# Kernel optimization log

Hardware: AMD Instinct MI355X
Metric: run time of the kernel (lower is better)

The kernel has to match this reference:

```python
import jax, jax.numpy as jnp
import numpy as np

N = 100000      # nodes
E = 3200000     # edges (avg degree 32)
IN_DIM = 256
OUT_DIM = 256


def setup_inputs() -> dict:
    key = jax.random.key(0)
    k1, k2, k3, k4, k5, k6 = jax.random.split(key, 6)
    row = jax.random.randint(k1, (E,), 0, N, dtype=jnp.int32)
    col = jax.random.randint(k2, (E,), 0, N, dtype=jnp.int32)
    vals = jax.random.uniform(k3, (E,), dtype=jnp.float32)
    x = jax.random.normal(k4, (N, IN_DIM), dtype=jnp.float32)
    W = jax.random.normal(k5, (IN_DIM, OUT_DIM), dtype=jnp.float32) * (IN_DIM ** -0.5)
    b = jax.random.normal(k6, (OUT_DIM,), dtype=jnp.float32) * 0.01
    return {"row": row, "col": col, "vals": vals, "x": x, "W": W, "b": b}


def reference(row, col, vals, x, W, b):
    # H = A_hat @ x  (sparse COO matmul via gather + segment-sum scatter)
    gathered = vals[:, None] * x[col]              # [E, in_dim]
    agg = jax.ops.segment_sum(gathered, row, num_segments=N)  # [N, in_dim]
    # Dense linear: agg @ W + b
    return agg @ W + b                             # [N, out_dim]
```

## Files before the change

### kernel.cpp

```cpp
#include <hip/hip_runtime.h>

#define IN_DIM 256
#define OUT_DIM 256
#define NBITS 8
#define CHUNK 8192
#define CAP 13056
#define VAL_SCALE 32767.0f
#define INV_VAL_SCALE (1.0f / 32767.0f)

typedef __attribute__((ext_vector_type(8))) short bf16x8;
typedef __attribute__((ext_vector_type(4))) float f32x4;

static __device__ __forceinline__ unsigned short f2bf(float f) {
    unsigned int u = __float_as_uint(f);
    u = (u + 0x7FFFu + ((u >> 16) & 1u)) >> 16;
    return (unsigned short)u;
}

__global__ __launch_bounds__(256) void prep_kernel(const float* __restrict__ W,
                                                   unsigned short* __restrict__ Wb,
                                                   int* __restrict__ cursor, int nb) {
    int blk = blockIdx.x;
    int t = threadIdx.x;
    if (blk < 256) {
        int idx = blk * 256 + t;
        int k = idx >> 8, c = idx & 255;
        Wb[(c >> 4) * 4096 + (k >> 3) * 128 + (c & 15) * 8 + (k & 7)] = f2bf(W[idx]);
    } else {
        for (int i = t; i < nb; i += 256) cursor[i] = i * CAP;
    }
}

__global__ __launch_bounds__(512) void gemm_scatter_fused(
        const float* __restrict__ x, const unsigned short* __restrict__ Wb,
        unsigned short* __restrict__ y, int M,
        const int* __restrict__ row, const int* __restrict__ col,
        const float* __restrict__ vals, int* __restrict__ cursor,
        unsigned int* __restrict__ edge_p, unsigned char* __restrict__ rowloc,
        int E, int nb, int GB) {
    __shared__ int hist[512];
    __shared__ int gbase[512];
    __shared__ int cur[512];

    if (blockIdx.x < (unsigned)GB) {
        const int t = threadIdx.x;
        const int lane = t & 63;
        const int wid = t >> 6;
        const int wr = wid >> 2;
        const int wc = wid & 3;
        const int r0 = blockIdx.x * 128 + wr * 64;
        const int c0 = wc * 64;

        f32x4 acc[4][4];
#pragma unroll
        for (int m = 0; m < 4; ++m)
#pragma unroll
            for (int n = 0; n < 4; ++n) acc[m][n] = (f32x4){0.f, 0.f, 0.f, 0.f};

        const int arow_off = lane & 15;
        const int kgrp = lane >> 4;

#pragma unroll
        for (int step = 0; step < 8; ++step) {
            const int k0 = step * 32 + kgrp * 8;
            bf16x8 a[4], bfr[4];
#pragma unroll
            for (int m = 0; m < 4; ++m) {
                int rr = r0 + m * 16 + arow_off;
                rr = min(rr, M - 1);
                const float* xr = x + (size_t)rr * IN_DIM + k0;
                float4 f0 = *reinterpret_cast<const float4*>(xr);
                float4 f1 = *reinterpret_cast<const float4*>(xr + 4);
                a[m][0] = (short)f2bf(f0.x); a[m][1] = (short)f2bf(f0.y);
                a[m][2] = (short)f2bf(f0.z); a[m][3] = (short)f2bf(f0.w);
                a[m][4] = (short)f2bf(f1.x); a[m][5] = (short)f2bf(f1.y);
                a[m][6] = (short)f2bf(f1.z); a[m][7] = (short)f2bf(f1.w);
            }
#pragma unroll
            for (int n = 0; n < 4; ++n) {
                int nbk = wc * 4 + n;
                bfr[n] = *reinterpret_cast<const bf16x8*>(
                    Wb + (size_t)nbk * 4096 + (step * 4 + kgrp) * 128 + arow_off * 8);
            }
#pragma unroll
            for (int m = 0; m < 4; ++m)
#pragma unroll
                for (int n = 0; n < 4; ++n)
                    acc[m][n] = __builtin_amdgcn_mfma_f32_16x16x32_bf16(a[m], bfr[n], acc[m][n], 0, 0, 0);
        }

#pragma unroll
        for (int m = 0; m < 4; ++m) {
            int rbase = r0 + m * 16 + kgrp * 4;
#pragma unroll
            for (int i = 0; i < 4; ++i) {
                int rr = rbase + i;
                if (rr < M) {
                    unsigned short* yr = y + (size_t)rr * OUT_DIM + c0 + arow_off;
#pragma unroll
                    for (int n = 0; n < 4; ++n) yr[n * 16] = f2bf(acc[m][n][i]);
                }
            }
        }
    } else {
        const int t = threadIdx.x;
        const int base_e = (blockIdx.x - GB) * CHUNK;
        for (int i = t; i < nb; i += 512) { hist[i] = 0; cur[i] = 0; }
        __syncthreads();
#pragma unroll
        for (int i = 0; i < CHUNK / 512; ++i) {
            int e = base_e + i * 512 + t;
            if (e < E) atomicAdd(&hist[row[e] >> NBITS], 1);
        }
        __syncthreads();
        for (int i = t; i < nb; i += 512) {
            int c = hist[i];
            if (c > 0) gbase[i] = atomicAdd(&cursor[i], c);
        }
        __syncthreads();
#pragma unroll
        for (int i = 0; i < CHUNK / 512; ++i) {
            int e = base_e + i * 512 + t;
            if (e < E) {
                int r = row[e];
                int bk = r >> NBITS;
                int loc = atomicAdd(&cur[bk], 1);
                int dest = gbase[bk] + loc;
                unsigned int vq = (unsigned int)(vals[e] * VAL_SCALE + 0.5f);
                edge_p[dest] = ((unsigned int)col[e] << 15) | vq;
                rowloc[dest] = (unsigned char)(r & 255);
            }
        }
    }
}

__global__ __launch_bounds__(512) void bucket_to_csr(const int* __restrict__ cursor,
                                                     unsigned int* __restrict__ edge_p,
                                                     const unsigned char* __restrict__ rowloc,
                                                     int2* __restrict__ row_se, int N, int nb) {
    __shared__ unsigned int ep[CAP];
    __shared__ unsigned char rl[CAP];
    __shared__ int cnt[256];
    __shared__ int cur[256];
    __shared__ int fin[256];
    __shared__ int wsum[4];
    const int t = threadIdx.x;
    const int b = blockIdx.x;
    const int gb = b * CAP;
    int m = cursor[b] - gb;
    if (m > CAP) m = CAP;
    if (t < 256) cnt[t] = 0;
    __syncthreads();
    for (int i = t; i < m; i += 512) {
        ep[i] = edge_p[gb + i];
        unsigned char r = rowloc[gb + i];
        rl[i] = r;
        atomicAdd(&cnt[r], 1);
    }
    __syncthreads();
    int pcv = 0, incl = 0;
    const int lane = t & 63;
    const int w = t >> 6;
    if (t < 256) {
        pcv = (cnt[t] + 3) & ~3;
        incl = pcv;
#pragma unroll
        for (int off = 1; off < 64; off <<= 1) {
            int u = __shfl_up(incl, off, 64);
            if (lane >= off) incl += u;
        }
        if (lane == 63) wsum[w] = incl;
    }
    __syncthreads();
    if (t < 256) {
        int wp = 0;
        for (int k = 0; k < w; ++k) wp += wsum[k];
        int excl = wp + incl - pcv;
        cur[t] = excl;
        fin[t] = excl + pcv;
        const int baseRow = b << NBITS;
        if (t < N - baseRow)
            row_se[baseRow + t] = make_int2(gb + excl, gb + excl + pcv);
    }
    __syncthreads();
    for (int i = t; i < m; i += 512) {
        int r = rl[i];
        int pos = atomicAdd(&cur[r], 1);
        edge_p[gb + pos] = ep[i];
    }
    __syncthreads();
    if (t < 256) {
        for (int pos = cur[t]; pos < fin[t]; ++pos)
            edge_p[gb + pos] = 0u;
    }
}

__global__ __launch_bounds__(256) void aggregate_rows_bf16(const int2* __restrict__ row_se,
                                                           const unsigned int* __restrict__ edge_p,
                                                           const unsigned short* __restrict__ y,
                                                           const float* __restrict__ b,
                                                           float* __restrict__ out, int N) {
    const int lane = threadIdx.x & 63;
    const int w = threadIdx.x >> 6;
    const int r = blockIdx.x * 4 + w;
    if (r >= N) return;

    const int2 se = row_se[r];
    const int start = se.x;
    const int end = se.y;
    const int half = lane >> 5;
    const int d0 = (lane & 31) * 8;

    float acc[8];
#pragma unroll
    for (int i = 0; i < 8; ++i) acc[i] = 0.f;

    int j = start;
    for (; j + 8 <= end; j += 8) {
        uint4 mp = *reinterpret_cast<const uint4*>(edge_p + j + half * 4);
        float v0 = (float)(mp.x & 0x7fffu) * INV_VAL_SCALE;
        float v1 = (float)(mp.y & 0x7fffu) * INV_VAL_SCALE;
        float v2 = (float)(mp.z & 0x7fffu) * INV_VAL_SCALE;
        float v3 = (float)(mp.w & 0x7fffu) * INV_VAL_SCALE;
        uint4 u0 = *reinterpret_cast<const uint4*>(y + ((size_t)(mp.x >> 15)) * OUT_DIM + d0);
        uint4 u1 = *reinterpret_cast<const uint4*>(y + ((size_t)(mp.y >> 15)) * OUT_DIM + d0);
        uint4 u2 = *reinterpret_cast<const uint4*>(y + ((size_t)(mp.z >> 15)) * OUT_DIM + d0);
        uint4 u3 = *reinterpret_cast<const uint4*>(y + ((size_t)(mp.w >> 15)) * OUT_DIM + d0);
        acc[0] += v0 * __uint_as_float(u0.x << 16);
        acc[1] += v0 * __uint_as_float(u0.x & 0xffff0000u);
        acc[2] += v0 * __uint_as_float(u0.y << 16);
        acc[3] += v0 * __uint_as_float(u0.y & 0xffff0000u);
        acc[4] += v0 * __uint_as_float(u0.z << 16);
        acc[5] += v0 * __uint_as_float(u0.z & 0xffff0000u);
        acc[6] += v0 * __uint_as_float(u0.w << 16);
        acc[7] += v0 * __uint_as_float(u0.w & 0xffff0000u);
        acc[0] += v1 * __uint_as_float(u1.x << 16);
        acc[1] += v1 * __uint_as_float(u1.x & 0xffff0000u);
        acc[2] += v1 * __uint_as_float(u1.y << 16);
        acc[3] += v1 * __uint_as_float(u1.y & 0xffff0000u);
        acc[4] += v1 * __uint_as_float(u1.z << 16);
        acc[5] += v1 * __uint_as_float(u1.z & 0xffff0000u);
        acc[6] += v1 * __uint_as_float(u1.w << 16);
        acc[7] += v1 * __uint_as_float(u1.w & 0xffff0000u);
        acc[0] += v2 * __uint_as_float(u2.x << 16);
        acc[1] += v2 * __uint_as_float(u2.x & 0xffff0000u);
        acc[2] += v2 * __uint_as_float(u2.y << 16);
        acc[3] += v2 * __uint_as_float(u2.y & 0xffff0000u);
        acc[4] += v2 * __uint_as_float(u2.z << 16);
        acc[5] += v2 * __uint_as_float(u2.z & 0xffff0000u);
        acc[6] += v2 * __uint_as_float(u2.w << 16);
        acc[7] += v2 * __uint_as_float(u2.w & 0xffff0000u);
        acc[0] += v3 * __uint_as_float(u3.x << 16);
        acc[1] += v3 * __uint_as_float(u3.x & 0xffff0000u);
        acc[2] += v3 * __uint_as_float(u3.y << 16);
        acc[3] += v3 * __uint_as_float(u3.y & 0xffff0000u);
        acc[4] += v3 * __uint_as_float(u3.z << 16);
        acc[5] += v3 * __uint_as_float(u3.z & 0xffff0000u);
        acc[6] += v3 * __uint_as_float(u3.w << 16);
        acc[7] += v3 * __uint_as_float(u3.w & 0xffff0000u);
    }
    if (j < end) {
        uint2 mp = *reinterpret_cast<const uint2*>(edge_p + j + half * 2);
        float v0 = (float)(mp.x & 0x7fffu) * INV_VAL_SCALE;
        float v1 = (float)(mp.y & 0x7fffu) * INV_VAL_SCALE;
        uint4 u0 = *reinterpret_cast<const uint4*>(y + ((size_t)(mp.x >> 15)) * OUT_DIM + d0);
        uint4 u1 = *reinterpret_cast<const uint4*>(y + ((size_t)(mp.y >> 15)) * OUT_DIM + d0);
        acc[0] += v0 * __uint_as_float(u0.x << 16);
        acc[1] += v0 * __uint_as_float(u0.x & 0xffff0000u);
        acc[2] += v0 * __uint_as_float(u0.y << 16);
        acc[3] += v0 * __uint_as_float(u0.y & 0xffff0000u);
        acc[4] += v0 * __uint_as_float(u0.z << 16);
        acc[5] += v0 * __uint_as_float(u0.z & 0xffff0000u);
        acc[6] += v0 * __uint_as_float(u0.w << 16);
        acc[7] += v0 * __uint_as_float(u0.w & 0xffff0000u);
        acc[0] += v1 * __uint_as_float(u1.x << 16);
        acc[1] += v1 * __uint_as_float(u1.x & 0xffff0000u);
        acc[2] += v1 * __uint_as_float(u1.y << 16);
        acc[3] += v1 * __uint_as_float(u1.y & 0xffff0000u);
        acc[4] += v1 * __uint_as_float(u1.z << 16);
        acc[5] += v1 * __uint_as_float(u1.z & 0xffff0000u);
        acc[6] += v1 * __uint_as_float(u1.w << 16);
        acc[7] += v1 * __uint_as_float(u1.w & 0xffff0000u);
    }

#pragma unroll
    for (int i = 0; i < 8; ++i) acc[i] += __shfl_xor(acc[i], 32, 64);

    if (half == 0) {
        float4 b0 = *reinterpret_cast<const float4*>(b + d0);
        float4 b1 = *reinterpret_cast<const float4*>(b + d0 + 4);
        float4 o0 = make_float4(acc[0] + b0.x, acc[1] + b0.y, acc[2] + b0.z, acc[3] + b0.w);
        float4 o1 = make_float4(acc[4] + b1.x, acc[5] + b1.y, acc[6] + b1.z, acc[7] + b1.w);
        float* op = out + (size_t)r * OUT_DIM + d0;
        *reinterpret_cast<float4*>(op) = o0;
        *reinterpret_cast<float4*>(op + 4) = o1;
    }
}

extern "C" void kernel_launch(void* const* d_in, const int* in_sizes, int n_in,
                              void* d_out, int out_size, void* d_ws, size_t ws_size,
                              hipStream_t stream) {
    const int*   row  = (const int*)d_in[0];
    const int*   col  = (const int*)d_in[1];
    const float* vals = (const float*)d_in[2];
    const float* x    = (const float*)d_in[3];
    const float* W    = (const float*)d_in[4];
    const float* b    = (const float*)d_in[5];
    const int E = in_sizes[0];
    const int N = in_sizes[3] / IN_DIM;
    const int nb = (N + 255) >> NBITS;

    float* out = (float*)d_out;

    char* ws = (char*)d_ws;
    size_t off = 0;
    unsigned short* y = (unsigned short*)(ws + off);  off += (size_t)N * OUT_DIM * 2;
    off = (off + 255) & ~(size_t)255;
    unsigned short* Wb = (unsigned short*)(ws + off); off += (size_t)IN_DIM * OUT_DIM * 2;
    off = (off + 255) & ~(size_t)255;
    unsigned int* edge_p = (unsigned int*)(ws + off); off += (size_t)nb * CAP * 4;
    unsigned char* rowloc = (unsigned char*)(ws + off); off += (size_t)nb * CAP;
    off = (off + 255) & ~(size_t)255;
    int* cursor = (int*)(ws + off);                   off += (size_t)nb * 4;
    off = (off + 255) & ~(size_t)255;
    int2* row_se = (int2*)(ws + off);                 off += (size_t)N * 8;

    const int GB = (N + 127) / 128;
    const int SB = (E + CHUNK - 1) / CHUNK;

    prep_kernel<<<257, 256, 0, stream>>>(W, Wb, cursor, nb);

    gemm_scatter_fused<<<GB + SB, 512, 0, stream>>>(x, Wb, y, N,
                                                    row, col, vals, cursor,
                                                    edge_p, rowloc, E, nb, GB);

    bucket_to_csr<<<nb, 512, 0, stream>>>(cursor, edge_p, rowloc, row_se, N, nb);

    aggregate_rows_bf16<<<(N + 3) / 4, 256, 0, stream>>>(row_se, edge_p, y, b, out, N);
}
```

Before: 410.3 us.

## Regroup kernel fusion: pair GEMM with bucket-to-CSR instead of with scatter

The edge-bucketing scatter becomes its own kernel. It now reads row/col/vals once into registers instead of reading row twice. The GEMM is fused with the per-bucket CSR permutation, so the compute-heavy MFMA blocks run beside the memory-bound permute blocks. The aggregation kernel moves to 1024-thread blocks handling 16 rows each. Risks: the GEMM blocks now use a block shape with a large LDS footprint, which may cut occupancy, and register pressure in the scatter kernel grows.

```diff
diff --git a/kernel.cpp b/kernel.cpp
--- a/kernel.cpp
+++ b/kernel.cpp
@@ -31,24 +31,128 @@
     }
 }
 
-__global__ __launch_bounds__(512) void gemm_scatter_fused(
-        const float* __restrict__ x, const unsigned short* __restrict__ Wb,
-        unsigned short* __restrict__ y, int M,
-        const int* __restrict__ row, const int* __restrict__ col,
-        const float* __restrict__ vals, int* __restrict__ cursor,
-        unsigned int* __restrict__ edge_p, unsigned char* __restrict__ rowloc,
-        int E, int nb, int GB) {
+__global__ __launch_bounds__(512) void bucket_scatter(const int* __restrict__ row,
+                                                      const int* __restrict__ col,
+                                                      const float* __restrict__ vals,
+                                                      int* __restrict__ cursor,
+                                                      unsigned int* __restrict__ edge_p,
+                                                      unsigned char* __restrict__ rowloc,
+                                                      int E, int nb) {
     __shared__ int hist[512];
     __shared__ int gbase[512];
     __shared__ int cur[512];
-
-    if (blockIdx.x < (unsigned)GB) {
-        const int t = threadIdx.x;
+    const int t = threadIdx.x;
+    const int base_e = blockIdx.x * CHUNK;
+
+    int bk_s[CHUNK / 512];
+    unsigned int pay_s[CHUNK / 512];
+    unsigned char rl_s[CHUNK / 512];
+
+    for (int i = t; i < nb; i += 512) { hist[i] = 0; cur[i] = 0; }
+    __syncthreads();
+#pragma unroll
+    for (int i = 0; i < CHUNK / 512; ++i) {
+        int e = base_e + i * 512 + t;
+        if (e < E) {
+            int r = row[e];
+            int bk = r >> NBITS;
+            unsigned int vq = (unsigned int)(vals[e] * VAL_SCALE + 0.5f);
+            bk_s[i] = bk;
+            pay_s[i] = ((unsigned int)col[e] << 15) | vq;
+            rl_s[i] = (unsigned char)(r & 255);
+            atomicAdd(&hist[bk], 1);
+        } else {
+            bk_s[i] = -1;
+        }
+    }
+    __syncthreads();
+    for (int i = t; i < nb; i += 512) {
+        int c = hist[i];
+        if (c > 0) gbase[i] = atomicAdd(&cursor[i], c);
+    }
+    __syncthreads();
+#pragma unroll
+    for (int i = 0; i < CHUNK / 512; ++i) {
+        int bk = bk_s[i];
+        if (bk >= 0) {
+            int loc = atomicAdd(&cur[bk], 1);
+            int dest = gbase[bk] + loc;
+            edge_p[dest] = pay_s[i];
+            rowloc[dest] = rl_s[i];
+        }
+    }
+}
+
+__global__ __launch_bounds__(512) void permute_gemm_fused(
+        const int* __restrict__ cursor, unsigned int* __restrict__ edge_p,
+        const unsigned char* __restrict__ rowloc, int2* __restrict__ row_se,
+        int N, int nb,
+        const float* __restrict__ x, const unsigned short* __restrict__ Wb,
+        unsigned short* __restrict__ y, int M) {
+    __shared__ unsigned int ep[CAP];
+    __shared__ unsigned char rl[CAP];
+    __shared__ int cnt[256];
+    __shared__ int cur[256];
+    __shared__ int fin[256];
+    __shared__ int wsum[4];
+
+    const int t = threadIdx.x;
+    if (blockIdx.x < (unsigned)nb) {
+        const int b = blockIdx.x;
+        const int gb = b * CAP;
+        int m = cursor[b] - gb;
+        if (m > CAP) m = CAP;
+        if (t < 256) cnt[t] = 0;
+        __syncthreads();
+        for (int i = t; i < m; i += 512) {
+            ep[i] = edge_p[gb + i];
+            unsigned char r = rowloc[gb + i];
+            rl[i] = r;
+            atomicAdd(&cnt[r], 1);
+        }
+        __syncthreads();
+        int pcv = 0, incl = 0;
+        const int lane = t & 63;
+        const int w = t >> 6;
+        if (t < 256) {
+            pcv = (cnt[t] + 3) & ~3;
+            incl = pcv;
+#pragma unroll
+            for (int off = 1; off < 64; off <<= 1) {
+                int u = __shfl_up(incl, off, 64);
+                if (lane >= off) incl += u;
+            }
+            if (lane == 63) wsum[w] = incl;
+        }
+        __syncthreads();
+        if (t < 256) {
+            int wp = 0;
+            for (int k = 0; k < w; ++k) wp += wsum[k];
+            int excl = wp + incl - pcv;
+            cur[t] = excl;
+            fin[t] = excl + pcv;
+            const int baseRow = b << NBITS;
+            if (t < N - baseRow)
+                row_se[baseRow + t] = make_int2(gb + excl, gb + excl + pcv);
+        }
+        __syncthreads();
+        for (int i = t; i < m; i += 512) {
+            int r = rl[i];
+            int pos = atomicAdd(&cur[r], 1);
+            edge_p[gb + pos] = ep[i];
+        }
+        __syncthreads();
+        if (t < 256) {
+            for (int pos = cur[t]; pos < fin[t]; ++pos)
+                edge_p[gb + pos] = 0u;
+        }
+    } else {
+        const int gblk = blockIdx.x - nb;
         const int lane = t & 63;
         const int wid = t >> 6;
         const int wr = wid >> 2;
         const int wc = wid & 3;
-        const int r0 = blockIdx.x * 128 + wr * 64;
+        const int r0 = gblk * 128 + wr * 64;
         const int c0 = wc * 64;
 
         f32x4 acc[4][4];
@@ -102,107 +206,17 @@
                 }
             }
         }
-    } else {
-        const int t = threadIdx.x;
-        const int base_e = (blockIdx.x - GB) * CHUNK;
-        for (int i = t; i < nb; i += 512) { hist[i] = 0; cur[i] = 0; }
-        __syncthreads();
-#pragma unroll
-        for (int i = 0; i < CHUNK / 512; ++i) {
-            int e = base_e + i * 512 + t;
-            if (e < E) atomicAdd(&hist[row[e] >> NBITS], 1);
-        }
-        __syncthreads();
-        for (int i = t; i < nb; i += 512) {
-            int c = hist[i];
-            if (c > 0) gbase[i] = atomicAdd(&cursor[i], c);
-        }
-        __syncthreads();
-#pragma unroll
-        for (int i = 0; i < CHUNK / 512; ++i) {
-            int e = base_e + i * 512 + t;
-            if (e < E) {
-                int r = row[e];
-                int bk = r >> NBITS;
-                int loc = atomicAdd(&cur[bk], 1);
-                int dest = gbase[bk] + loc;
-                unsigned int vq = (unsigned int)(vals[e] * VAL_SCALE + 0.5f);
-                edge_p[dest] = ((unsigned int)col[e] << 15) | vq;
-                rowloc[dest] = (unsigned char)(r & 255);
-            }
-        }
-    }
-}
-
-__global__ __launch_bounds__(512) void bucket_to_csr(const int* __restrict__ cursor,
-                                                     unsigned int* __restrict__ edge_p,
-                                                     const unsigned char* __restrict__ rowloc,
-                                                     int2* __restrict__ row_se, int N, int nb) {
-    __shared__ unsigned int ep[CAP];
-    __shared__ unsigned char rl[CAP];
-    __shared__ int cnt[256];
-    __shared__ int cur[256];
-    __shared__ int fin[256];
-    __shared__ int wsum[4];
-    const int t = threadIdx.x;
-    const int b = blockIdx.x;
-    const int gb = b * CAP;
-    int m = cursor[b] - gb;
-    if (m > CAP) m = CAP;
-    if (t < 256) cnt[t] = 0;
-    __syncthreads();
-    for (int i = t; i < m; i += 512) {
-        ep[i] = edge_p[gb + i];
-        unsigned char r = rowloc[gb + i];
-        rl[i] = r;
-        atomicAdd(&cnt[r], 1);
-    }
-    __syncthreads();
-    int pcv = 0, incl = 0;
-    const int lane = t & 63;
-    const int w = t >> 6;
-    if (t < 256) {
-        pcv = (cnt[t] + 3) & ~3;
-        incl = pcv;
-#pragma unroll
-        for (int off = 1; off < 64; off <<= 1) {
-            int u = __shfl_up(incl, off, 64);
-            if (lane >= off) incl += u;
-        }
-        if (lane == 63) wsum[w] = incl;
-    }
-    __syncthreads();
-    if (t < 256) {
-        int wp = 0;
-        for (int k = 0; k < w; ++k) wp += wsum[k];
-        int excl = wp + incl - pcv;
-        cur[t] = excl;
-        fin[t] = excl + pcv;
-        const int baseRow = b << NBITS;
-        if (t < N - baseRow)
-            row_se[baseRow + t] = make_int2(gb + excl, gb + excl + pcv);
-    }
-    __syncthreads();
-    for (int i = t; i < m; i += 512) {
-        int r = rl[i];
-        int pos = atomicAdd(&cur[r], 1);
-        edge_p[gb + pos] = ep[i];
-    }
-    __syncthreads();
-    if (t < 256) {
-        for (int pos = cur[t]; pos < fin[t]; ++pos)
-            edge_p[gb + pos] = 0u;
-    }
-}
-
-__global__ __launch_bounds__(256) void aggregate_rows_bf16(const int2* __restrict__ row_se,
-                                                           const unsigned int* __restrict__ edge_p,
-                                                           const unsigned short* __restrict__ y,
-                                                           const float* __restrict__ b,
-                                                           float* __restrict__ out, int N) {
+    }
+}
+
+__global__ __launch_bounds__(1024) void aggregate_rows_bf16(const int2* __restrict__ row_se,
+                                                            const unsigned int* __restrict__ edge_p,
+                                                            const unsigned short* __restrict__ y,
+                                                            const float* __restrict__ b,
+                                                            float* __restrict__ out, int N) {
     const int lane = threadIdx.x & 63;
     const int w = threadIdx.x >> 6;
-    const int r = blockIdx.x * 4 + w;
+    const int r = blockIdx.x * 16 + w;
     if (r >= N) return;
 
     const int2 se = row_se[r];
@@ -330,11 +344,11 @@
 
     prep_kernel<<<257, 256, 0, stream>>>(W, Wb, cursor, nb);
 
-    gemm_scatter_fused<<<GB + SB, 512, 0, stream>>>(x, Wb, y, N,
-                                                    row, col, vals, cursor,
-                                                    edge_p, rowloc, E, nb, GB);
-
-    bucket_to_csr<<<nb, 512, 0, stream>>>(cursor, edge_p, rowloc, row_se, N, nb);
-
-    aggregate_rows_bf16<<<(N + 3) / 4, 256, 0, stream>>>(row_se, edge_p, y, b, out, N);
-}
+    bucket_scatter<<<SB, 512, 0, stream>>>(row, col, vals, cursor,
+                                           edge_p, rowloc, E, nb);
+
+    permute_gemm_fused<<<nb + GB, 512, 0, stream>>>(cursor, edge_p, rowloc, row_se,
+                                                    N, nb, x, Wb, y, N);
+
+    aggregate_rows_bf16<<<(N + 15) / 16, 1024, 0, stream>>>(row_se, edge_p, y, b, out, N);
+}
```

Result: faster. 387.5 us (-5.6%).
